# Optimization experiments

Hardware: AMD Instinct MI355X
Metric: run time of the kernel (lower is better)

Reference implementation:

```python
import jax, jax.numpy as jnp
import numpy as np

K = 3      # kernel size
S = 1      # stride
P = (K - 1) // 2  # same padding


def setup_inputs() -> dict:
    key = jax.random.key(0)
    k1, k2, k3 = jax.random.split(key, 3)
    x = jax.random.normal(k1, (8, 64, 128, 128), dtype=jnp.float32)
    C2, CIN = 96, 64 * K * K
    # Linear(c1*k^2, c2): weight (c2, c1*k^2), bias (c2,)
    W = jax.random.normal(k2, (C2, CIN), dtype=jnp.float32) / np.sqrt(CIN)
    b = jax.random.normal(k3, (C2,), dtype=jnp.float32) * 0.01
    return {"x": x, "W": W, "b": b}


def _unfold(x):
    # torch nn.Unfold(kernel_size=K, stride=S, padding=P):
    # output (B, C*K*K, L), feature index = c*K*K + ki*K + kj
    B, C, H, Wd = x.shape
    xp = jnp.pad(x, ((0, 0), (0, 0), (P, P), (P, P)))
    Ho = (H + 2 * P - K) // S + 1
    Wo = (Wd + 2 * P - K) // S + 1
    # small fixed K*K loop (9 slices), channel-major ordering matches torch
    patches = jnp.stack(
        [xp[:, :, i:i + (Ho - 1) * S + 1:S, j:j + (Wo - 1) * S + 1:S]
         for i in range(K) for j in range(K)],
        axis=2,
    )  # (B, C, K*K, Ho, Wo)
    return patches.reshape(B, C * K * K, Ho * Wo)


def reference(x, W, b):
    feat = _unfold(x)                      # (B, C*K*K, P)
    feat = jnp.swapaxes(feat, 1, 2)        # (B, P, C*K*K)  == Rearrange 'n c p -> n p c'
    return feat @ W.T + b                  # (B, P, c2)
```

## Files before the change

kernel.cpp:

```cpp
#include <hip/hip_runtime.h>
#include <hip/hip_bf16.h>
#include <stdint.h>


typedef __bf16 bf16t;
typedef __bf16 bf16x8 __attribute__((ext_vector_type(8)));
typedef float  f32x4  __attribute__((ext_vector_type(4)));

#define CIN   64
#define COUT  96
#define HH    128
#define WW    128
#define KTOT  576
#define NCH   18
#define XROW  (130 * 32)
#define XTOT  (4 * XROW)

__device__ __forceinline__ int swz8(int px) { return ((px >> 2) & 7) ^ ((px & 3) << 1); }

__device__ __forceinline__ uint32_t pack2(float lo, float hi) {
    uint16_t a = __builtin_bit_cast(uint16_t, (__bf16)lo);
    uint16_t b = __builtin_bit_cast(uint16_t, (__bf16)hi);
    return ((uint32_t)b << 16) | (uint32_t)a;
}

__global__ __launch_bounds__(256) void prep_w_kernel(
    const float* __restrict__ W, bf16t* __restrict__ Wp)
{
    int idx = blockIdx.x * 256 + threadIdx.x;
    if (idx >= NCH * COUT * 32) return;
    int ch  = idx / (COUT * 32);
    int rem = idx - ch * (COUT * 32);
    int n = rem >> 5, cc = rem & 31;
    int r = ch >> 1, half = ch & 1;
    Wp[idx] = (bf16t)W[n * KTOT + (half * 32 + cc) * 9 + r];
}

__global__ __launch_bounds__(512, 4) void conv_kernel(
    const float* __restrict__ x, const bf16t* __restrict__ Wp,
    const float* __restrict__ bias, float* __restrict__ out)
{
    __shared__ __align__(16) uint32_t Xs[XTOT];

    const int tid  = threadIdx.x;
    const int lane = tid & 63;
    const int wave = tid >> 6;
    const int lrow = lane & 15;
    const int quad = lane >> 4;
    const int wn   = wave & 1;
    const int wm   = wave >> 1;

    const int bb  = blockIdx.x & 7;
    const int orp = blockIdx.x >> 3;

    const bf16t* wp_n = Wp + (size_t)(wn * 48 + lrow) * 32 + quad * 8;

    bf16x8 bcur[3], bnxt[3];
    #pragma unroll
    for (int nt = 0; nt < 3; ++nt)
        bcur[nt] = *(const bf16x8*)(wp_n + nt * 512);

    uint4* X4 = (uint4*)Xs;
    #pragma unroll
    for (int i = 0; i < 9; ++i) {
        int idx = tid + 512 * i;
        if (idx < XTOT / 4) X4[idx] = (uint4){0u, 0u, 0u, 0u};
    }
    __syncthreads();

    const float* xb = x + (size_t)bb * CIN * HH * WW;
    #pragma unroll
    for (int it = 0; it < 8; ++it) {
        int g  = tid + 512 * it;
        int j0 = (g & 31) * 4;
        int cp = (g >> 5) & 31;
        int rh = g >> 10;
        int ii = orp * 2 - 1 + rh;
        if ((unsigned)ii < (unsigned)HH) {
            const float* s0 = xb + ((size_t)(2 * cp) * HH + ii) * WW + j0;
            float4 v0 = *(const float4*)s0;
            float4 v1 = *(const float4*)(s0 + HH * WW);
            float e0[4] = {v0.x, v0.y, v0.z, v0.w};
            float e1[4] = {v1.x, v1.y, v1.z, v1.w};
            #pragma unroll
            for (int u = 0; u < 4; ++u) {
                int px  = 1 + j0 + u;
                int cdw = (cp & 3) | ((((cp >> 2) ^ swz8(px)) & 7) << 2);
                Xs[rh * XROW + px * 32 + cdw] = pack2(e0[u], e1[u]);
            }
        }
    }
    __syncthreads();

    f32x4 acc[4][3];
    #pragma unroll
    for (int a = 0; a < 4; ++a)
        #pragma unroll
        for (int nt = 0; nt < 3; ++nt)
            acc[a][nt] = (f32x4){0.f, 0.f, 0.f, 0.f};

    #pragma unroll
    for (int ch = 0; ch < NCH; ++ch) {
        if (ch < NCH - 1) {
            #pragma unroll
            for (int nt = 0; nt < 3; ++nt)
                bnxt[nt] = *(const bf16x8*)(wp_n + (size_t)(ch + 1) * 3072 + nt * 512);
        }
        const int ki = ch / 6, kj = (ch % 6) >> 1, half = ch & 1;
        bf16x8 afr[4];
        #pragma unroll
        for (int a = 0; a < 4; ++a) {
            int mb   = wm * 64 + a * 16;
            int slab = (mb >> 7) + ki;
            int p    = (mb & 127) + lrow + kj;
            int blk  = (half * 4 + quad) ^ swz8(p);
            afr[a] = *(const bf16x8*)&Xs[slab * XROW + p * 32 + blk * 4];
        }
        #pragma unroll
        for (int a = 0; a < 4; ++a)
            #pragma unroll
            for (int nt = 0; nt < 3; ++nt)
                acc[a][nt] = __builtin_amdgcn_mfma_f32_16x16x32_bf16(
                    afr[a], bcur[nt], acc[a][nt], 0, 0, 0);
        #pragma unroll
        for (int nt = 0; nt < 3; ++nt) bcur[nt] = bnxt[nt];
    }

    float bv[3];
    #pragma unroll
    for (int nt = 0; nt < 3; ++nt) bv[nt] = bias[wn * 48 + nt * 16 + lrow];

    float* outp = out + ((size_t)bb * 16384 + (size_t)orp * 256) * COUT + wn * 48;
    #pragma unroll
    for (int a = 0; a < 4; ++a) {
        #pragma unroll
        for (int rg = 0; rg < 4; ++rg) {
            int mm = wm * 64 + a * 16 + quad * 4 + rg;
            float* rowp = outp + (size_t)mm * COUT;
            #pragma unroll
            for (int nt = 0; nt < 3; ++nt)
                rowp[nt * 16 + lrow] = acc[a][nt][rg] + bv[nt];
        }
    }
}

extern "C" void kernel_launch(void* const* d_in, const int* in_sizes, int n_in,
                              void* d_out, int out_size, void* d_ws, size_t ws_size,
                              hipStream_t stream) {
    const float* x    = (const float*)d_in[0];
    const float* W    = (const float*)d_in[1];
    const float* bias = (const float*)d_in[2];
    float* out = (float*)d_out;
    bf16t* Wp  = (bf16t*)d_ws;

    hipLaunchKernelGGL(prep_w_kernel, dim3((NCH * COUT * 32 + 255) / 256), dim3(256), 0, stream,
                       W, Wp);
    hipLaunchKernelGGL(conv_kernel, dim3(512), dim3(512), 0, stream,
                       x, Wp, bias, out);
}
```

Measured before the change: 109.9 us.

## Split conv into one-output-row blocks with 256 threads and register-staged row loads

Each block now computes a single output row (128 pixels) with 4 waves instead of two rows with 8 waves, doubling the grid to 1024 blocks and shrinking LDS to 3 input rows. Input rows are loaded into registers with a simple double buffer so the global load of the next row overlaps packing and storing the current one. Only the padding columns are zeroed rather than the whole buffer, which also removes a barrier. The aim is more resident blocks and better latency hiding, but the input halo is now re-read for 3 rows per output row instead of 4 per 2, so global input traffic rises.

```diff
diff --git a/kernel.cpp b/kernel.cpp
--- a/kernel.cpp
+++ b/kernel.cpp
@@ -14,7 +14,6 @@
 #define KTOT  576
 #define NCH   18
 #define XROW  (130 * 32)
-#define XTOT  (4 * XROW)
 
 __device__ __forceinline__ int swz8(int px) { return ((px >> 2) & 7) ^ ((px & 3) << 1); }
 
@@ -36,11 +35,11 @@
     Wp[idx] = (bf16t)W[n * KTOT + (half * 32 + cc) * 9 + r];
 }
 
-__global__ __launch_bounds__(512, 4) void conv_kernel(
+__global__ __launch_bounds__(256, 3) void conv_kernel(
     const float* __restrict__ x, const bf16t* __restrict__ Wp,
     const float* __restrict__ bias, float* __restrict__ out)
 {
-    __shared__ __align__(16) uint32_t Xs[XTOT];
+    __shared__ __align__(16) uint32_t Xs[3 * XROW];
 
     const int tid  = threadIdx.x;
     const int lane = tid & 63;
@@ -50,8 +49,8 @@
     const int wn   = wave & 1;
     const int wm   = wave >> 1;
 
-    const int bb  = blockIdx.x & 7;
-    const int orp = blockIdx.x >> 3;
+    const int bb = blockIdx.x & 7;
+    const int oi = blockIdx.x >> 3;
 
     const bf16t* wp_n = Wp + (size_t)(wn * 48 + lrow) * 32 + quad * 8;
 
@@ -60,33 +59,58 @@
     for (int nt = 0; nt < 3; ++nt)
         bcur[nt] = *(const bf16x8*)(wp_n + nt * 512);
 
-    uint4* X4 = (uint4*)Xs;
-    #pragma unroll
-    for (int i = 0; i < 9; ++i) {
-        int idx = tid + 512 * i;
-        if (idx < XTOT / 4) X4[idx] = (uint4){0u, 0u, 0u, 0u};
+    if (tid < 192) {
+        int s = tid >> 6, c129 = (tid >> 5) & 1, dw = tid & 31;
+        Xs[s * XROW + (c129 ? 129 : 0) * 32 + dw] = 0u;
     }
-    __syncthreads();
 
     const float* xb = x + (size_t)bb * CIN * HH * WW;
+    const int j0  = (tid & 31) * 4;
+    const int cp0 = tid >> 5;
+    float4 vb[2][8];
+
+    {
+        int ii = oi - 1;
+        if (ii >= 0) {
+            #pragma unroll
+            for (int q = 0; q < 4; ++q) {
+                const float* s0 = xb + ((size_t)(2 * (q * 8 + cp0)) * HH + ii) * WW + j0;
+                vb[0][2 * q]     = *(const float4*)s0;
+                vb[0][2 * q + 1] = *(const float4*)(s0 + HH * WW);
+            }
+        } else {
+            #pragma unroll
+            for (int i = 0; i < 8; ++i) vb[0][i] = (float4){0.f, 0.f, 0.f, 0.f};
+        }
+    }
     #pragma unroll
-    for (int it = 0; it < 8; ++it) {
-        int g  = tid + 512 * it;
-        int j0 = (g & 31) * 4;
-        int cp = (g >> 5) & 31;
-        int rh = g >> 10;
-        int ii = orp * 2 - 1 + rh;
-        if ((unsigned)ii < (unsigned)HH) {
-            const float* s0 = xb + ((size_t)(2 * cp) * HH + ii) * WW + j0;
-            float4 v0 = *(const float4*)s0;
-            float4 v1 = *(const float4*)(s0 + HH * WW);
-            float e0[4] = {v0.x, v0.y, v0.z, v0.w};
-            float e1[4] = {v1.x, v1.y, v1.z, v1.w};
+    for (int s = 0; s < 3; ++s) {
+        if (s < 2) {
+            int ii = oi + s;
+            if (ii < HH) {
+                #pragma unroll
+                for (int q = 0; q < 4; ++q) {
+                    const float* s0 = xb + ((size_t)(2 * (q * 8 + cp0)) * HH + ii) * WW + j0;
+                    vb[(s + 1) & 1][2 * q]     = *(const float4*)s0;
+                    vb[(s + 1) & 1][2 * q + 1] = *(const float4*)(s0 + HH * WW);
+                }
+            } else {
+                #pragma unroll
+                for (int i = 0; i < 8; ++i) vb[(s + 1) & 1][i] = (float4){0.f, 0.f, 0.f, 0.f};
+            }
+        }
+        #pragma unroll
+        for (int q = 0; q < 4; ++q) {
+            int cpp = q * 8 + cp0;
+            float e0[4] = {vb[s & 1][2 * q].x, vb[s & 1][2 * q].y,
+                           vb[s & 1][2 * q].z, vb[s & 1][2 * q].w};
+            float e1[4] = {vb[s & 1][2 * q + 1].x, vb[s & 1][2 * q + 1].y,
+                           vb[s & 1][2 * q + 1].z, vb[s & 1][2 * q + 1].w};
             #pragma unroll
             for (int u = 0; u < 4; ++u) {
                 int px  = 1 + j0 + u;
-                int cdw = (cp & 3) | ((((cp >> 2) ^ swz8(px)) & 7) << 2);
-                Xs[rh * XROW + px * 32 + cdw] = pack2(e0[u], e1[u]);
+                int cdw = (cpp & 3) | ((((cpp >> 2) ^ swz8(px)) & 7) << 2);
+                Xs[s * XROW + px * 32 + cdw] = pack2(e0[u], e1[u]);
             }
         }
     }
@@ -110,11 +134,9 @@
         bf16x8 afr[4];
         #pragma unroll
         for (int a = 0; a < 4; ++a) {
-            int mb   = wm * 64 + a * 16;
-            int slab = (mb >> 7) + ki;
-            int p    = (mb & 127) + lrow + kj;
-            int blk  = (half * 4 + quad) ^ swz8(p);
-            afr[a] = *(const bf16x8*)&Xs[slab * XROW + p * 32 + blk * 4];
+            int p   = wm * 64 + a * 16 + lrow + kj;
+            int blk = (half * 4 + quad) ^ swz8(p);
+            afr[a] = *(const bf16x8*)&Xs[ki * XROW + p * 32 + blk * 4];
         }
         #pragma unroll
         for (int a = 0; a < 4; ++a)
@@ -130,7 +152,7 @@
     #pragma unroll
     for (int nt = 0; nt < 3; ++nt) bv[nt] = bias[wn * 48 + nt * 16 + lrow];
 
-    float* outp = out + ((size_t)bb * 16384 + (size_t)orp * 256) * COUT + wn * 48;
+    float* outp = out + ((size_t)bb * 16384 + (size_t)oi * 128) * COUT + wn * 48;
     #pragma unroll
     for (int a = 0; a < 4; ++a) {
         #pragma unroll
@@ -155,6 +177,6 @@
 
     hipLaunchKernelGGL(prep_w_kernel, dim3((NCH * COUT * 32 + 255) / 256), dim3(256), 0, stream,
                        W, Wp);
-    hipLaunchKernelGGL(conv_kernel, dim3(512), dim3(512), 0, stream,
+    hipLaunchKernelGGL(conv_kernel, dim3(1024), dim3(256), 0, stream,
                        x, Wp, bias, out);
 }
```

After: 111.7 us. No clear change (+1.6%).
